# Kernel tuning notes

Hardware: AMD Instinct MI355X
Metric: run time of the kernel (lower is better)

## Reference

```python
import jax, jax.numpy as jnp
import numpy as np

V, E, H = 50000, 100, 128
B, S = 16, 4096
NUM_LEVELS = int(np.log2(S)) + 1  # 13; level l has S >> l nodes
# gate order in the 5-gate stack: i, f_l, f_r, o, u
XMAP = jnp.array([0, 1, 1, 2, 3])


def setup_inputs() -> dict:
    key = jax.random.key(0)
    ks = jax.random.split(key, 9)
    sE = 1.0 / np.sqrt(E)
    sH = 1.0 / np.sqrt(H)
    return {
        "embedding": jax.random.normal(ks[0], (V, E), jnp.float32) * 0.1,
        "W_x": jax.random.normal(ks[1], (4, H, E), jnp.float32) * sE,   # (i,f,o,u) x-projections
        "b_x": jax.random.normal(ks[2], (4, H), jnp.float32) * sE,
        "U_l": jax.random.normal(ks[3], (5, H, H), jnp.float32) * sH,   # (u_i_l,u_f_ll,u_f_rr,u_o_l,u_u_l) applied to h_left
        "b_l": jax.random.normal(ks[4], (5, H), jnp.float32) * sH,
        "U_r": jax.random.normal(ks[5], (5, H, H), jnp.float32) * sH,   # (u_i_r,u_f_lr,u_f_rl,u_o_r,u_u_r) applied to h_right
        "b_r": jax.random.normal(ks[6], (5, H), jnp.float32) * sH,
        "input_seq": jax.random.randint(ks[7], (B, S), 0, V, jnp.int32),
        "dep_tags": jax.random.randint(ks[8], (NUM_LEVELS - 1, S // 2), 0, S, jnp.int32),
    }


def _level_step(x5, h_l, h_r, c_l, c_r, U_l, b_l, U_r, b_r):
    # x5: [B,N,5,H] per-gate x contributions (w_*(x) incl. bias)
    pre = (x5
           + jnp.einsum('bnk,ghk->bngh', h_l, U_l) + b_l
           + jnp.einsum('bnk,ghk->bngh', h_r, U_r) + b_r)  # [B,N,5,H]
    i   = jax.nn.sigmoid(pre[:, :, 0])
    f_l = jax.nn.sigmoid(pre[:, :, 1])
    f_r = jax.nn.sigmoid(pre[:, :, 2])
    o   = jax.nn.sigmoid(pre[:, :, 3])
    u   = jnp.tanh(pre[:, :, 4])
    c = i * u + f_l * c_l + f_r * c_r
    h = o * jnp.tanh(c)
    return h, c


def reference(embedding, W_x, b_x, U_l, b_l, U_r, b_r, input_seq, dep_tags):
    b, s = input_seq.shape
    emb = embedding[input_seq]  # [B,S,E]
    xg = jnp.einsum('bse,ghe->bsgh', emb, W_x) + b_x  # [B,S,4,H]

    # level 0: every leaf is a token, children are zero
    z = jnp.zeros((b, s, xg.shape[-1]), xg.dtype)
    h, c = _level_step(xg[:, :, XMAP, :], z, z, z, z, U_l, b_l, U_r, b_r)

    for l in range(1, NUM_LEVELS):
        n = s >> l
        dep = dep_tags[l - 1, :n]                # token position re-embedded at each internal node
        x5 = xg[:, dep][:, :, XMAP, :]           # [B,N,5,H]
        hp = h.reshape(b, n, 2, -1)              # node i's children are (2i, 2i+1)
        cp = c.reshape(b, n, 2, -1)
        h, c = _level_step(x5, hp[:, :, 0], hp[:, :, 1], cp[:, :, 0], cp[:, :, 1],
                           U_l, b_l, U_r, b_r)
    return h[:, 0], c[:, 0]  # root (h, c): [B,H] each
```

## Files before the change

### kernel.cpp

```cpp
#include <hip/hip_runtime.h>
#include <hip/hip_bf16.h>

#define V_ 50000
#define E_ 100
#define H_ 128
#define B_ 16
#define S_ 4096

typedef unsigned short u16;
typedef unsigned int   u32;
typedef short bf16x8 __attribute__((ext_vector_type(8)));
typedef float f32x4  __attribute__((ext_vector_type(4)));

__device__ __forceinline__ float bf2f(u16 x) {
  return __uint_as_float(((u32)x) << 16);
}
__device__ __forceinline__ u16 f2bf(float x) {
  __hip_bfloat16 b = __float2bfloat16(x);
  return *reinterpret_cast<u16*>(&b);
}
__device__ __forceinline__ float sigm(float x) { return 1.0f / (1.0f + __expf(-x)); }
__device__ __forceinline__ float tanh_f(float x) {
  float e = __expf(2.0f * x);
  return 1.0f - 2.0f / (e + 1.0f);
}

#define PREP_N0 (V_ * 128)
#define PREP_N1 65536
#define PREP_N2 163840
#define PREP_N3 640
__global__ __launch_bounds__(256) void prep_all(
    const float* __restrict__ emb, const float* __restrict__ Wx,
    const float* __restrict__ Ul, const float* __restrict__ Ur,
    const float* __restrict__ bl, const float* __restrict__ br,
    const float* __restrict__ bx,
    u16* __restrict__ embB, u16* __restrict__ Bx, u16* __restrict__ Bu,
    float* __restrict__ bxs, float* __restrict__ bd)
{
  int i = blockIdx.x * 256 + threadIdx.x;
  if (i < PREP_N0) {
    int k = i & 127, t = i >> 7;
    embB[i] = (k < E_) ? f2bf(emb[t * E_ + k]) : (u16)0;
    return;
  }
  i -= PREP_N0;
  if (i < PREP_N1) {
    int j = i & 7, l = (i >> 3) & 63, s = (i >> 9) & 3, t = i >> 11;
    int k = s * 32 + (l >> 4) * 8 + j;
    int o = t * 16 + (l & 15);
    Bx[i] = (k < E_) ? f2bf(Wx[o * E_ + k]) : (u16)0;
    return;
  }
  i -= PREP_N1;
  if (i < PREP_N2) {
    int j = i & 7, l = (i >> 3) & 63, s = (i >> 9) & 7, t = i >> 12;
    int k = s * 32 + (l >> 4) * 8 + j;
    int gh = t * 16 + (l & 15);
    float v = (k < 128) ? Ul[gh * 128 + k] : Ur[gh * 128 + (k - 128)];
    Bu[i] = f2bf(v);
    return;
  }
  i -= PREP_N2;
  if (i < 512) {
    int g = i >> 7, hh = i & 127;
    int lg = (g == 0) ? 0 : (g == 1) ? 1 : (g == 2) ? 3 : 4;
    bxs[i] = bx[i] + bl[lg * 128 + hh] + br[lg * 128 + hh];
    return;
  }
  i -= 512;
  if (i < 128) bd[i] = (bl[256 + i] + br[256 + i]) - (bl[128 + i] + br[128 + i]);
}

#define XLDS 514
__global__ __launch_bounds__(512) void xg_mfma(
    const u16* __restrict__ embB, const u16* __restrict__ Bx,
    const float* __restrict__ bxs, const int* __restrict__ seq,
    ushort4* __restrict__ xg, u16* __restrict__ h0, u16* __restrict__ c0)
{
  __shared__ u16 lds[32 * XLDS];
  const int w = threadIdx.x >> 6, lane = threadIdx.x & 63;
  const int quad = lane >> 4, l15 = lane & 15;
  const int m0 = blockIdx.x * 32;

  f32x4 acc[2][4];
  #pragma unroll
  for (int r = 0; r < 2; ++r)
    #pragma unroll
    for (int t = 0; t < 4; ++t) acc[r][t] = (f32x4){0.f, 0.f, 0.f, 0.f};

  int tok0 = seq[m0 + l15];
  int tok1 = seq[m0 + 16 + l15];
  const u16* a0p = embB + (size_t)tok0 * 128 + quad * 8;
  const u16* a1p = embB + (size_t)tok1 * 128 + quad * 8;

  #pragma unroll
  for (int s = 0; s < 4; ++s) {
    bf16x8 a0 = *reinterpret_cast<const bf16x8*>(a0p + s * 32);
    bf16x8 a1 = *reinterpret_cast<const bf16x8*>(a1p + s * 32);
    #pragma unroll
    for (int ti = 0; ti < 4; ++ti) {
      int t = w * 4 + ti;
      bf16x8 b = *reinterpret_cast<const bf16x8*>(Bx + ((size_t)(t * 4 + s) * 64 + lane) * 8);
      acc[0][ti] = __builtin_amdgcn_mfma_f32_16x16x32_bf16(a0, b, acc[0][ti], 0, 0, 0);
      acc[1][ti] = __builtin_amdgcn_mfma_f32_16x16x32_bf16(a1, b, acc[1][ti], 0, 0, 0);
    }
  }

  const int g = w >> 1;
  #pragma unroll
  for (int ti = 0; ti < 4; ++ti) {
    int o = (w * 4 + ti) * 16 + l15;
    float bxo = bxs[o];
    int hhw = (w & 1) * 64 + ti * 16 + l15;
    #pragma unroll
    for (int r = 0; r < 2; ++r)
      #pragma unroll
      for (int reg = 0; reg < 4; ++reg) {
        int mrow = r * 16 + quad * 4 + reg;
        lds[mrow * XLDS + hhw * 4 + g] = f2bf(acc[r][ti][reg] + bxo);
      }
  }
  __syncthreads();

  #pragma unroll
  for (int i = 0; i < 8; ++i) {
    int pidx = i * 512 + threadIdx.x;
    int m = pidx >> 7, hh = pidx & 127;
    ushort4 v = *reinterpret_cast<const ushort4*>(&lds[m * XLDS + hh * 4]);
    size_t gm = (size_t)(m0 + m);
    xg[gm * 128 + hh] = v;
    float c = sigm(bf2f(v.x)) * tanh_f(bf2f(v.w));
    float h = sigm(bf2f(v.z)) * tanh_f(c);
    h0[gm * 128 + hh] = f2bf(h);
    c0[gm * 128 + hh] = f2bf(c);
  }
}

__global__ __launch_bounds__(512) void level_mfma64(
    const ushort4* __restrict__ xg4, const int* __restrict__ deprow,
    const u16* __restrict__ Bu, const float* __restrict__ bd,
    const u16* __restrict__ hPrev, const u16* __restrict__ cPrev,
    u16* __restrict__ hOut, u16* __restrict__ cOut, int n, int ln2n)
{
  const int w = threadIdx.x >> 6, lane = threadIdx.x & 63;
  const int quad = lane >> 4, l15 = lane & 15;
  const int hh = w * 16 + l15;
  const int m0 = blockIdx.x * 64;

  ushort4 xv[16];
  #pragma unroll
  for (int i = 0; i < 16; ++i) {
    int m = m0 + (i >> 2) * 16 + quad * 4 + (i & 3);
    int j = m & (n - 1);
    int b = m >> ln2n;
    xv[i] = xg4[((size_t)b * S_ + deprow[j]) * 128 + hh];
  }

  f32x4 acc[4][5];
  #pragma unroll
  for (int r = 0; r < 4; ++r)
    #pragma unroll
    for (int g = 0; g < 5; ++g) acc[r][g] = (f32x4){0.f, 0.f, 0.f, 0.f};

  const u16* ap = hPrev + (size_t)(m0 + l15) * 256 + quad * 8;

  #pragma unroll
  for (int s = 0; s < 8; ++s) {
    bf16x8 a[4];
    #pragma unroll
    for (int r = 0; r < 4; ++r)
      a[r] = *reinterpret_cast<const bf16x8*>(ap + (size_t)r * 16 * 256 + s * 32);
    #pragma unroll
    for (int g = 0; g < 5; ++g) {
      int t = g * 8 + w;
      bf16x8 b = *reinterpret_cast<const bf16x8*>(Bu + ((size_t)(t * 8 + s) * 64 + lane) * 8);
      #pragma unroll
      for (int r = 0; r < 4; ++r)
        acc[r][g] = __builtin_amdgcn_mfma_f32_16x16x32_bf16(a[r], b, acc[r][g], 0, 0, 0);
    }
  }

  float bdv = bd[hh];
  #pragma unroll
  for (int i = 0; i < 16; ++i) {
    int r = i >> 2, reg = i & 3;
    int m = m0 + r * 16 + quad * 4 + reg;
    ushort4 v = xv[i];
    float x0 = bf2f(v.x), x1 = bf2f(v.y), x2 = bf2f(v.z), x3 = bf2f(v.w);
    float cl = bf2f(cPrev[(size_t)m * 256 + hh]);
    float cr = bf2f(cPrev[(size_t)m * 256 + 128 + hh]);
    float pi  = acc[r][0][reg] + x0;
    float pfl = acc[r][1][reg] + x1;
    float pfr = acc[r][2][reg] + x1 + bdv;
    float po  = acc[r][3][reg] + x2;
    float pu  = acc[r][4][reg] + x3;
    float c = sigm(pi) * tanh_f(pu) + sigm(pfl) * cl + sigm(pfr) * cr;
    float h = sigm(po) * tanh_f(c);
    hOut[(size_t)m * 128 + hh] = f2bf(h);
    cOut[(size_t)m * 128 + hh] = f2bf(c);
  }
}

__global__ __launch_bounds__(512) void level_mfma(
    const ushort4* __restrict__ xg4, const int* __restrict__ deprow,
    const u16* __restrict__ Bu, const float* __restrict__ bd,
    const u16* __restrict__ hPrev, const u16* __restrict__ cPrev,
    u16* __restrict__ hOut, u16* __restrict__ cOut, int n, int ln2n)
{
  const int w = threadIdx.x >> 6, lane = threadIdx.x & 63;
  const int quad = lane >> 4, l15 = lane & 15;
  const int hh = w * 16 + l15;
  const int m0 = blockIdx.x * 32;

  ushort4 xv[8];
  float clv[8], crv[8];
  #pragma unroll
  for (int i = 0; i < 8; ++i) {
    int m = m0 + (i >> 2) * 16 + quad * 4 + (i & 3);
    int j = m & (n - 1);
    int b = m >> ln2n;
    int dj = deprow[j];
    xv[i] = xg4[((size_t)b * S_ + dj) * 128 + hh];
    clv[i] = bf2f(cPrev[(size_t)m * 256 + hh]);
    crv[i] = bf2f(cPrev[(size_t)m * 256 + 128 + hh]);
  }

  f32x4 acc[2][5];
  #pragma unroll
  for (int r = 0; r < 2; ++r)
    #pragma unroll
    for (int g = 0; g < 5; ++g) acc[r][g] = (f32x4){0.f, 0.f, 0.f, 0.f};

  const u16* a0p = hPrev + (size_t)(m0 + l15) * 256 + quad * 8;
  const u16* a1p = a0p + 16 * 256;

  #pragma unroll
  for (int s = 0; s < 8; ++s) {
    bf16x8 a0 = *reinterpret_cast<const bf16x8*>(a0p + s * 32);
    bf16x8 a1 = *reinterpret_cast<const bf16x8*>(a1p + s * 32);
    #pragma unroll
    for (int g = 0; g < 5; ++g) {
      int t = g * 8 + w;
      bf16x8 b = *reinterpret_cast<const bf16x8*>(Bu + ((size_t)(t * 8 + s) * 64 + lane) * 8);
      acc[0][g] = __builtin_amdgcn_mfma_f32_16x16x32_bf16(a0, b, acc[0][g], 0, 0, 0);
      acc[1][g] = __builtin_amdgcn_mfma_f32_16x16x32_bf16(a1, b, acc[1][g], 0, 0, 0);
    }
  }

  float bdv = bd[hh];
  #pragma unroll
  for (int i = 0; i < 8; ++i) {
    int r = i >> 2, reg = i & 3;
    int m = m0 + r * 16 + quad * 4 + reg;
    ushort4 v = xv[i];
    float x0 = bf2f(v.x), x1 = bf2f(v.y), x2 = bf2f(v.z), x3 = bf2f(v.w);
    float pi  = acc[r][0][reg] + x0;
    float pfl = acc[r][1][reg] + x1;
    float pfr = acc[r][2][reg] + x1 + bdv;
    float po  = acc[r][3][reg] + x2;
    float pu  = acc[r][4][reg] + x3;
    float c = sigm(pi) * tanh_f(pu) + sigm(pfl) * clv[i] + sigm(pfr) * crv[i];
    float h = sigm(po) * tanh_f(c);
    hOut[(size_t)m * 128 + hh] = f2bf(h);
    cOut[(size_t)m * 128 + hh] = f2bf(c);
  }
}

__global__ __launch_bounds__(512) void deep_fused(
    const ushort4* __restrict__ xg4, const int* __restrict__ dep,
    const u16* __restrict__ Bu, const float* __restrict__ bd,
    const u16* __restrict__ h6, const u16* __restrict__ c6,
    float* __restrict__ out)
{
  __shared__ u16  hls[2][32 * 136];
  __shared__ float cls[2][32 * 128];
  const int b = blockIdx.x;
  const int w = threadIdx.x >> 6, lane = threadIdx.x & 63;
  const int quad = lane >> 4, l15 = lane & 15;
  const int hh = w * 16 + l15;

  const float bdv = bd[hh];

  {
    ushort4 xv[2][4];
    float clv[2][4], crv[2][4];
    #pragma unroll
    for (int r = 0; r < 2; ++r)
      #pragma unroll
      for (int reg = 0; reg < 4; ++reg) {
        int j = r * 16 + quad * 4 + reg;
        int dj = dep[6 * 2048 + j];
        xv[r][reg] = xg4[((size_t)b * S_ + dj) * 128 + hh];
        clv[r][reg] = bf2f(c6[(size_t)(b * 32 + j) * 256 + hh]);
        crv[r][reg] = bf2f(c6[(size_t)(b * 32 + j) * 256 + 128 + hh]);
      }

    f32x4 acc[2][5];
    #pragma unroll
    for (int r = 0; r < 2; ++r)
      #pragma unroll
      for (int g = 0; g < 5; ++g) acc[r][g] = (f32x4){0.f, 0.f, 0.f, 0.f};

    #pragma unroll
    for (int s = 0; s < 8; ++s) {
      const u16* ap = h6 + (size_t)(b * 32 + l15) * 256 + s * 32 + quad * 8;
      bf16x8 a0 = *reinterpret_cast<const bf16x8*>(ap);
      bf16x8 a1 = *reinterpret_cast<const bf16x8*>(ap + 16 * 256);
      #pragma unroll
      for (int g = 0; g < 5; ++g) {
        int t = g * 8 + w;
        bf16x8 bb = *reinterpret_cast<const bf16x8*>(Bu + ((size_t)(t * 8 + s) * 64 + lane) * 8);
        acc[0][g] = __builtin_amdgcn_mfma_f32_16x16x32_bf16(a0, bb, acc[0][g], 0, 0, 0);
        acc[1][g] = __builtin_amdgcn_mfma_f32_16x16x32_bf16(a1, bb, acc[1][g], 0, 0, 0);
      }
    }

    #pragma unroll
    for (int r = 0; r < 2; ++r)
      #pragma unroll
      for (int reg = 0; reg < 4; ++reg) {
        int j = r * 16 + quad * 4 + reg;
        ushort4 v = xv[r][reg];
        float x0 = bf2f(v.x), x1 = bf2f(v.y), x2 = bf2f(v.z), x3 = bf2f(v.w);
        float pi  = acc[r][0][reg] + x0;
        float pfl = acc[r][1][reg] + x1;
        float pfr = acc[r][2][reg] + x1 + bdv;
        float po  = acc[r][3][reg] + x2;
        float pu  = acc[r][4][reg] + x3;
        float c = sigm(pi) * tanh_f(pu) + sigm(pfl) * clv[r][reg] + sigm(pfr) * crv[r][reg];
        float h = sigm(po) * tanh_f(c);
        hls[0][j * 136 + hh] = f2bf(h);
        cls[0][j * 128 + hh] = c;
      }
  }
  __syncthreads();

  ushort4 xvc[4];
  #pragma unroll
  for (int reg = 0; reg < 4; ++reg)
    xvc[reg] = xg4[((size_t)b * S_ + dep[7 * 2048 + quad * 4 + reg]) * 128 + hh];

  int pb = 0;
  for (int lvl = 8; lvl <= 12; ++lvl) {
    int nb = 4096 >> lvl;

    ushort4 xvn[4];
    if (lvl < 12) {
      int nbn = 2048 >> lvl;
      #pragma unroll
      for (int reg = 0; reg < 4; ++reg) {
        int j = quad * 4 + reg;
        if (j < nbn)
          xvn[reg] = xg4[((size_t)b * S_ + dep[lvl * 2048 + j]) * 128 + hh];
      }
    }

    f32x4 acc[5];
    #pragma unroll
    for (int g = 0; g < 5; ++g) acc[g] = (f32x4){0.f, 0.f, 0.f, 0.f};

    #pragma unroll
    for (int s = 0; s < 8; ++s) {
      int child = 2 * l15 + (s >= 4 ? 1 : 0);
      int kk = (s & 3) * 32 + quad * 8;
      bf16x8 a = *reinterpret_cast<const bf16x8*>(&hls[pb][child * 136 + kk]);
      #pragma unroll
      for (int g = 0; g < 5; ++g) {
        int t = g * 8 + w;
        bf16x8 bb = *reinterpret_cast<const bf16x8*>(Bu + ((size_t)(t * 8 + s) * 64 + lane) * 8);
        acc[g] = __builtin_amdgcn_mfma_f32_16x16x32_bf16(a, bb, acc[g], 0, 0, 0);
      }
    }

    #pragma unroll
    for (int reg = 0; reg < 4; ++reg) {
      int j = quad * 4 + reg;
      if (j < nb) {
        ushort4 v = xvc[reg];
        float x0 = bf2f(v.x), x1 = bf2f(v.y), x2 = bf2f(v.z), x3 = bf2f(v.w);
        float cl = cls[pb][(2 * j) * 128 + hh];
        float cr = cls[pb][(2 * j + 1) * 128 + hh];
        float pi  = acc[0][reg] + x0;
        float pfl = acc[1][reg] + x1;
        float pfr = acc[2][reg] + x1 + bdv;
        float po  = acc[3][reg] + x2;
        float pu  = acc[4][reg] + x3;
        float c = sigm(pi) * tanh_f(pu) + sigm(pfl) * cl + sigm(pfr) * cr;
        float h = sigm(po) * tanh_f(c);
        hls[pb ^ 1][j * 136 + hh] = f2bf(h);
        cls[pb ^ 1][j * 128 + hh] = c;
        if (lvl == 12) {
          out[b * 128 + hh] = h;
          out[2048 + b * 128 + hh] = c;
        }
      }
    }
    __syncthreads();
    pb ^= 1;
    #pragma unroll
    for (int reg = 0; reg < 4; ++reg) xvc[reg] = xvn[reg];
  }
}

extern "C" void kernel_launch(void* const* d_in, const int* in_sizes, int n_in,
                              void* d_out, int out_size, void* d_ws, size_t ws_size,
                              hipStream_t stream)
{
  const float* emb = (const float*)d_in[0];
  const float* Wx  = (const float*)d_in[1];
  const float* bx  = (const float*)d_in[2];
  const float* Ul  = (const float*)d_in[3];
  const float* bl  = (const float*)d_in[4];
  const float* Ur  = (const float*)d_in[5];
  const float* br  = (const float*)d_in[6];
  const int* seq = (const int*)d_in[7];
  const int* dep = (const int*)d_in[8];

  char* p = (char*)d_ws;
  u16* embB = (u16*)p;    p += (size_t)V_ * 128 * 2;
  u16* BswX = (u16*)p;    p += 131072;
  u16* BswU = (u16*)p;    p += 327680;
  float* bxs = (float*)p; p += 2048;
  float* bd = (float*)p;  p += 2048;
  u16* xg = (u16*)p;      p += (size_t)B_ * S_ * 512 * 2;
  u16* h0 = (u16*)p;      p += (size_t)B_ * S_ * 128 * 2;
  u16* c0 = (u16*)p;      p += (size_t)B_ * S_ * 128 * 2;
  u16* hA = (u16*)p;      p += (size_t)32768 * 128 * 2;
  u16* cA = (u16*)p;      p += (size_t)32768 * 128 * 2;
  u16* hB = (u16*)p;      p += (size_t)16384 * 128 * 2;
  u16* cB = (u16*)p;      p += (size_t)16384 * 128 * 2;

  const int prep_tot = PREP_N0 + PREP_N1 + PREP_N2 + PREP_N3;
  prep_all<<<dim3((prep_tot + 255) / 256), dim3(256), 0, stream>>>(
      emb, Wx, Ul, Ur, bl, br, bx, embB, BswX, BswU, bxs, bd);

  xg_mfma<<<dim3(B_ * S_ / 32), dim3(512), 0, stream>>>(
      embB, BswX, bxs, seq, (ushort4*)xg, h0, c0);

  const ushort4* xg4 = (const ushort4*)xg;

  level_mfma64<<<dim3(32768 / 64), dim3(512), 0, stream>>>(
      xg4, dep, BswU, bd, h0, c0, hA, cA, 2048, 11);

  u16 *hp = hA, *ho = hB;
  u16 *cp = cA, *co = cB;
  for (int l = 2; l <= 3; ++l) {
    int n = S_ >> l;
    int Mtot = B_ * n;
    const int* deprow = dep + (size_t)(l - 1) * (S_ / 2);
    level_mfma64<<<dim3(Mtot / 64), dim3(512), 0, stream>>>(
        xg4, deprow, BswU, bd, hp, cp, ho, co, n, 12 - l);
    u16* th = hp; hp = ho; ho = th;
    u16* tc = cp; cp = co; co = tc;
  }
  for (int l = 4; l <= 6; ++l) {
    int n = S_ >> l;
    int Mtot = B_ * n;
    const int* deprow = dep + (size_t)(l - 1) * (S_ / 2);
    level_mfma<<<dim3(Mtot / 32), dim3(512), 0, stream>>>(
        xg4, deprow, BswU, bd, hp, cp, ho, co, n, 12 - l);
    u16* th = hp; hp = ho; ho = th;
    u16* tc = cp; cp = co; co = tc;
  }

  deep_fused<<<dim3(16), dim3(512), 0, stream>>>(
      xg4, dep, BswU, bd, hp, cp, (float*)d_out);
}
```

Before: 264.8 us.

## Fuse leaf level into level-1 kernel and fold level 6 into deep kernel

The leaf-level h/c computation moves out of the xg projection kernel and into a new level-1 kernel. That kernel recomputes leaf h and c from xg into LDS, so the h0/c0 global buffers are no longer written or read back. Separately, the level-6 launch is removed and deep_fused now starts from level-5 outputs, computing level 6 in LDS before the remaining levels. This saves global traffic and one launch, at the cost of larger LDS use in both kernels and more serial work per block in the 16-block deep kernel.

```diff
diff --git a/kernel.cpp b/kernel.cpp
--- a/kernel.cpp
+++ b/kernel.cpp
@@ -75,7 +75,7 @@
 __global__ __launch_bounds__(512) void xg_mfma(
     const u16* __restrict__ embB, const u16* __restrict__ Bx,
     const float* __restrict__ bxs, const int* __restrict__ seq,
-    ushort4* __restrict__ xg, u16* __restrict__ h0, u16* __restrict__ c0)
+    ushort4* __restrict__ xg)
 {
   __shared__ u16 lds[32 * XLDS];
   const int w = threadIdx.x >> 6, lane = threadIdx.x & 63;
@@ -127,12 +127,87 @@
     int pidx = i * 512 + threadIdx.x;
     int m = pidx >> 7, hh = pidx & 127;
     ushort4 v = *reinterpret_cast<const ushort4*>(&lds[m * XLDS + hh * 4]);
-    size_t gm = (size_t)(m0 + m);
-    xg[gm * 128 + hh] = v;
+    xg[(size_t)(m0 + m) * 128 + hh] = v;
+  }
+}
+
+__global__ __launch_bounds__(512) void level1_fused(
+    const ushort4* __restrict__ xg4, const int* __restrict__ deprow,
+    const u16* __restrict__ Bu, const float* __restrict__ bd,
+    u16* __restrict__ hOut, u16* __restrict__ cOut)
+{
+  __shared__ u16 hls[128 * 136];
+  __shared__ u16 cls[128 * 128];
+  const int w = threadIdx.x >> 6, lane = threadIdx.x & 63;
+  const int quad = lane >> 4, l15 = lane & 15;
+  const int hh = w * 16 + l15;
+  const int m0 = blockIdx.x * 64;
+
+  ushort4 xv[16];
+  #pragma unroll
+  for (int i = 0; i < 16; ++i) {
+    int m = m0 + (i >> 2) * 16 + quad * 4 + (i & 3);
+    int j = m & 2047;
+    int b = m >> 11;
+    xv[i] = xg4[((size_t)b * S_ + deprow[j]) * 128 + hh];
+  }
+
+  #pragma unroll
+  for (int i = 0; i < 32; ++i) {
+    int idx = i * 512 + threadIdx.x;
+    int lr = idx >> 7, ph = idx & 127;
+    ushort4 v = xg4[((size_t)(2 * m0) + lr) * 128 + ph];
     float c = sigm(bf2f(v.x)) * tanh_f(bf2f(v.w));
     float h = sigm(bf2f(v.z)) * tanh_f(c);
-    h0[gm * 128 + hh] = f2bf(h);
-    c0[gm * 128 + hh] = f2bf(c);
+    hls[lr * 136 + ph] = f2bf(h);
+    cls[lr * 128 + ph] = f2bf(c);
+  }
+  __syncthreads();
+
+  f32x4 acc[4][5];
+  #pragma unroll
+  for (int r = 0; r < 4; ++r)
+    #pragma unroll
+    for (int g = 0; g < 5; ++g) acc[r][g] = (f32x4){0.f, 0.f, 0.f, 0.f};
+
+  #pragma unroll
+  for (int s = 0; s < 8; ++s) {
+    bf16x8 a[4];
+    #pragma unroll
+    for (int r = 0; r < 4; ++r) {
+      int child = 2 * (r * 16 + l15) + (s >= 4 ? 1 : 0);
+      int kk = (s & 3) * 32 + quad * 8;
+      a[r] = *reinterpret_cast<const bf16x8*>(&hls[child * 136 + kk]);
+    }
+    #pragma unroll
+    for (int g = 0; g < 5; ++g) {
+      int t = g * 8 + w;
+      bf16x8 b = *reinterpret_cast<const bf16x8*>(Bu + ((size_t)(t * 8 + s) * 64 + lane) * 8);
+      #pragma unroll
+      for (int r = 0; r < 4; ++r)
+        acc[r][g] = __builtin_amdgcn_mfma_f32_16x16x32_bf16(a[r], b, acc[r][g], 0, 0, 0);
+    }
+  }
+
+  float bdv = bd[hh];
+  #pragma unroll
+  for (int i = 0; i < 16; ++i) {
+    int r = i >> 2, reg = i & 3;
+    int lm = r * 16 + quad * 4 + reg;
+    int m = m0 + lm;
+    ushort4 v = xv[i];
+    float x0 = bf2f(v.x), x1 = bf2f(v.y), x2 = bf2f(v.z), x3 = bf2f(v.w);
+    float cl = bf2f(cls[(2 * lm) * 128 + hh]);
+    float cr = bf2f(cls[(2 * lm + 1) * 128 + hh]);
+    float pi  = acc[r][0][reg] + x0;
+    float pfl = acc[r][1][reg] + x1;
+    float pfr = acc[r][2][reg] + x1 + bdv;
+    float po  = acc[r][3][reg] + x2;
+    float pu  = acc[r][4][reg] + x3;
+    float c = sigm(pi) * tanh_f(pu) + sigm(pfl) * cl + sigm(pfr) * cr;
+    float h = sigm(po) * tanh_f(c);
+    hOut[(size_t)m * 128 + hh] = f2bf(h);
+    cOut[(size_t)m * 128 + hh] = f2bf(c);
   }
 }
 
@@ -269,11 +344,11 @@
 __global__ __launch_bounds__(512) void deep_fused(
     const ushort4* __restrict__ xg4, const int* __restrict__ dep,
     const u16* __restrict__ Bu, const float* __restrict__ bd,
-    const u16* __restrict__ h6, const u16* __restrict__ c6,
+    const u16* __restrict__ h5, const u16* __restrict__ c5,
     float* __restrict__ out)
 {
-  __shared__ u16  hls[2][32 * 136];
-  __shared__ float cls[2][32 * 128];
+  __shared__ u16  hls[2][64 * 136];
+  __shared__ float cls[2][64 * 128];
   const int b = blockIdx.x;
   const int w = threadIdx.x >> 6, lane = threadIdx.x & 63;
   const int quad = lane >> 4, l15 = lane & 15;
@@ -282,36 +357,90 @@
   const float bdv = bd[hh];
 
   {
-    ushort4 xv[2][4];
-    float clv[2][4], crv[2][4];
-    #pragma unroll
-    for (int r = 0; r < 2; ++r)
-      #pragma unroll
-      for (int reg = 0; reg < 4; ++reg) {
-        int j = r * 16 + quad * 4 + reg;
-        int dj = dep[6 * 2048 + j];
-        xv[r][reg] = xg4[((size_t)b * S_ + dj) * 128 + hh];
-        clv[r][reg] = bf2f(c6[(size_t)(b * 32 + j) * 256 + hh]);
-        crv[r][reg] = bf2f(c6[(size_t)(b * 32 + j) * 256 + 128 + hh]);
-      }
-
-    f32x4 acc[2][5];
-    #pragma unroll
-    for (int r = 0; r < 2; ++r)
+    ushort4 xv[16];
+    #pragma unroll
+    for (int i = 0; i < 16; ++i) {
+      int j = (i >> 2) * 16 + quad * 4 + (i & 3);
+      xv[i] = xg4[((size_t)b * S_ + dep[5 * 2048 + j]) * 128 + hh];
+    }
+
+    f32x4 acc[4][5];
+    #pragma unroll
+    for (int r = 0; r < 4; ++r)
       #pragma unroll
       for (int g = 0; g < 5; ++g) acc[r][g] = (f32x4){0.f, 0.f, 0.f, 0.f};
 
+    const u16* ap = h5 + (size_t)(b * 64 + l15) * 256 + quad * 8;
+
     #pragma unroll
     for (int s = 0; s < 8; ++s) {
-      const u16* ap = h6 + (size_t)(b * 32 + l15) * 256 + s * 32 + quad * 8;
-      bf16x8 a0 = *reinterpret_cast<const bf16x8*>(ap);
-      bf16x8 a1 = *reinterpret_cast<const bf16x8*>(ap + 16 * 256);
+      bf16x8 a[4];
+      #pragma unroll
+      for (int r = 0; r < 4; ++r)
+        a[r] = *reinterpret_cast<const bf16x8*>(ap + (size_t)r * 16 * 256 + s * 32);
       #pragma unroll
       for (int g = 0; g < 5; ++g) {
         int t = g * 8 + w;
         bf16x8 bb = *reinterpret_cast<const bf16x8*>(Bu + ((size_t)(t * 8 + s) * 64 + lane) * 8);
-        acc[0][g] = __builtin_amdgcn_mfma_f32_16x16x32_bf16(a0, bb, acc[0][g], 0, 0, 0);
-        acc[1][g] = __builtin_amdgcn_mfma_f32_16x16x32_bf16(a1, bb, acc[1][g], 0, 0, 0);
+        #pragma unroll
+        for (int r = 0; r < 4; ++r)
+          acc[r][g] = __builtin_amdgcn_mfma_f32_16x16x32_bf16(a[r], bb, acc[r][g], 0, 0, 0);
+      }
+    }
+
+    #pragma unroll
+    for (int i = 0; i < 16; ++i) {
+      int r = i >> 2, reg = i & 3;
+      int lm = r * 16 + quad * 4 + reg;
+      int m = b * 64 + lm;
+      ushort4 v = xv[i];
+      float x0 = bf2f(v.x), x1 = bf2f(v.y), x2 = bf2f(v.z), x3 = bf2f(v.w);
+      float cl = bf2f(c5[(size_t)m * 256 + hh]);
+      float cr = bf2f(c5[(size_t)m * 256 + 128 + hh]);
+      float pi  = acc[r][0][reg] + x0;
+      float pfl = acc[r][1][reg] + x1;
+      float pfr = acc[r][2][reg] + x1 + bdv;
+      float po  = acc[r][3][reg] + x2;
+      float pu  = acc[r][4][reg] + x3;
+      float c = sigm(pi) * tanh_f(pu) + sigm(pfl) * cl + sigm(pfr) * cr;
+      float h = sigm(po) * tanh_f(c);
+      hls[0][lm * 136 + hh] = f2bf(h);
+      cls[0][lm * 128 + hh] = c;
+    }
+  }
+  __syncthreads();
+
+  {
+    ushort4 xv[2][4];
+    #pragma unroll
+    for (int r = 0; r < 2; ++r)
+      #pragma unroll
+      for (int reg = 0; reg < 4; ++reg) {
+        int j = r * 16 + quad * 4 + reg;
+        xv[r][reg] = xg4[((size_t)b * S_ + dep[6 * 2048 + j]) * 128 + hh];
+      }
+
+    f32x4 acc[2][5];
+    #pragma unroll
+    for (int r = 0; r < 2; ++r)
+      #pragma unroll
+      for (int g = 0; g < 5; ++g) acc[r][g] = (f32x4){0.f, 0.f, 0.f, 0.f};
+
+    #pragma unroll
+    for (int s = 0; s < 8; ++s) {
+      bf16x8 a[2];
+      #pragma unroll
+      for (int r = 0; r < 2; ++r) {
+        int child = 2 * (r * 16 + l15) + (s >= 4 ? 1 : 0);
+        int kk = (s & 3) * 32 + quad * 8;
+        a[r] = *reinterpret_cast<const bf16x8*>(&hls[0][child * 136 + kk]);
+      }
+      #pragma unroll
+      for (int g = 0; g < 5; ++g) {
+        int t = g * 8 + w;
+        bf16x8 bb = *reinterpret_cast<const bf16x8*>(Bu + ((size_t)(t * 8 + s) * 64 + lane) * 8);
+        acc[0][g] = __builtin_amdgcn_mfma_f32_16x16x32_bf16(a[0], bb, acc[0][g], 0, 0, 0);
+        acc[1][g] = __builtin_amdgcn_mfma_f32_16x16x32_bf16(a[1], bb, acc[1][g], 0, 0, 0);
       }
     }
 
@@ -322,15 +451,17 @@
         int j = r * 16 + quad * 4 + reg;
         ushort4 v = xv[r][reg];
         float x0 = bf2f(v.x), x1 = bf2f(v.y), x2 = bf2f(v.z), x3 = bf2f(v.w);
+        float cl = cls[0][(2 * j) * 128 + hh];
+        float cr = cls[0][(2 * j + 1) * 128 + hh];
         float pi  = acc[r][0][reg] + x0;
         float pfl = acc[r][1][reg] + x1;
         float pfr = acc[r][2][reg] + x1 + bdv;
         float po  = acc[r][3][reg] + x2;
         float pu  = acc[r][4][reg] + x3;
-        float c = sigm(pi) * tanh_f(pu) + sigm(pfl) * clv[r][reg] + sigm(pfr) * crv[r][reg];
+        float c = sigm(pi) * tanh_f(pu) + sigm(pfl) * cl + sigm(pfr) * cr;
         float h = sigm(po) * tanh_f(c);
-        hls[0][j * 136 + hh] = f2bf(h);
-        cls[0][j * 128 + hh] = c;
+        hls[1][j * 136 + hh] = f2bf(h);
+        cls[1][j * 128 + hh] = c;
       }
   }
   __syncthreads();
@@ -340,7 +471,7 @@
   for (int reg = 0; reg < 4; ++reg)
     xvc[reg] = xg4[((size_t)b * S_ + dep[7 * 2048 + quad * 4 + reg]) * 128 + hh];
 
-  int pb = 0;
+  int pb = 1;
   for (int lvl = 8; lvl <= 12; ++lvl) {
     int nb = 4096 >> lvl;
 
@@ -423,8 +554,6 @@
   float* bxs = (float*)p; p += 2048;
   float* bd = (float*)p;  p += 2048;
   u16* xg = (u16*)p;      p += (size_t)B_ * S_ * 512 * 2;
-  u16* h0 = (u16*)p;      p += (size_t)B_ * S_ * 128 * 2;
-  u16* c0 = (u16*)p;      p += (size_t)B_ * S_ * 128 * 2;
   u16* hA = (u16*)p;      p += (size_t)32768 * 128 * 2;
   u16* cA = (u16*)p;      p += (size_t)32768 * 128 * 2;
   u16* hB = (u16*)p;      p += (size_t)16384 * 128 * 2;
@@ -435,12 +564,12 @@
       emb, Wx, Ul, Ur, bl, br, bx, embB, BswX, BswU, bxs, bd);
 
   xg_mfma<<<dim3(B_ * S_ / 32), dim3(512), 0, stream>>>(
-      embB, BswX, bxs, seq, (ushort4*)xg, h0, c0);
+      embB, BswX, bxs, seq, (ushort4*)xg);
 
   const ushort4* xg4 = (const ushort4*)xg;
 
-  level_mfma64<<<dim3(32768 / 64), dim3(512), 0, stream>>>(
-      xg4, dep, BswU, bd, h0, c0, hA, cA, 2048, 11);
+  level1_fused<<<dim3(512), dim3(512), 0, stream>>>(
+      xg4, dep, BswU, bd, hA, cA);
 
   u16 *hp = hA, *ho = hB;
   u16 *cp = cA, *co = cB;
@@ -453,7 +582,7 @@
     u16* th = hp; hp = ho; ho = th;
     u16* tc = cp; cp = co; co = tc;
   }
-  for (int l = 4; l <= 6; ++l) {
+  for (int l = 4; l <= 5; ++l) {
     int n = S_ >> l;
     int Mtot = B_ * n;
     const int* deprow = dep + (size_t)(l - 1) * (S_ / 2);
```

Result: slower. 283.8 us (+7.2%).
